# Performance work log

Measured on AMD Instinct MI355X. Metric: run time of the kernel, lower is better.

The kernel has to match this reference:

```python
import jax, jax.numpy as jnp
import numpy as np

UPPER = 0.4
LOWER = 0.1
BG_RATIO = 1.0
NCLS = 20
BACKGROUND = NCLS
SIGMA = 10.0          # SmoothL1Loss(10)
MAX_POS = 2048        # fixed capacity for positive RoIs (jit-friendly)
NEGATIVE = -2
NEITHER = -1


def bbox_overlaps(b1, b2):
    """Pairwise IoU, py-faster-rcnn +1 pixel convention. b1 [L,4], b2 [M,4] -> [L,M]."""
    a1 = (b1[:, 2] - b1[:, 0] + 1.0) * (b1[:, 3] - b1[:, 1] + 1.0)  # [L]
    a2 = (b2[:, 2] - b2[:, 0] + 1.0) * (b2[:, 3] - b2[:, 1] + 1.0)  # [M]
    iw = jnp.clip(jnp.minimum(b1[:, None, 2], b2[None, :, 2]) -
                  jnp.maximum(b1[:, None, 0], b2[None, :, 0]) + 1.0, 0.0)
    ih = jnp.clip(jnp.minimum(b1[:, None, 3], b2[None, :, 3]) -
                  jnp.maximum(b1[:, None, 1], b2[None, :, 1]) + 1.0, 0.0)
    inter = iw * ih
    return inter / (a1[:, None] + a2[None, :] - inter)


def smooth_l1(d):
    s2 = SIGMA * SIGMA
    ad = jnp.abs(d)
    return jnp.where(ad < 1.0 / s2, 0.5 * s2 * d * d, ad - 0.5 / s2)


def match(pred, gt):
    """Faithful port of match(): same assignment order (upper -> gt-argmax -> lower)."""
    L = pred.shape[0]
    M = gt.shape[0]
    ov = bbox_overlaps(pred, gt)                       # [L, M]
    best_p = ov.max(axis=1)
    idx_p = ov.argmax(axis=1).astype(jnp.int32)
    ret = jnp.full((L,), NEITHER, dtype=jnp.int32)
    ret = jnp.where(best_p >= UPPER, idx_p, ret)
    idx_g = ov.argmax(axis=0)                          # [M] best roi per gt
    ret = ret.at[idx_g].set(jnp.arange(M, dtype=jnp.int32))
    ret = jnp.where(best_p < LOWER, NEGATIVE, ret)     # applied last, as in torch
    return ret


def reference(rois, cls_scores, bbox_deltas, gt_boxes, gt_cls):
    L, C = cls_scores.shape
    boxes = rois[:, 1:]                                # drop batch index column
    score_idx = jnp.argmax(cls_scores, axis=1)         # [L] predicted class per roi
    deltas = bbox_deltas.reshape(L, C, 4)
    deltas = jnp.take_along_axis(deltas, score_idx[:, None, None], axis=1)[:, 0, :]
    pred = boxes + deltas                              # [L, 4]
    gt = gt_boxes[0]                                   # [M, 4]

    matches = match(pred, gt)                          # [L] int32
    pos = matches >= 0
    neg = matches == NEGATIVE
    num_pos = pos.sum()

    # --- negative sampling: randperm(neg)[:bg_num], done via random ranks ---
    bg_num = jnp.round(num_pos.astype(jnp.float32) * BG_RATIO).astype(jnp.int32)
    u = jax.random.uniform(jax.random.key(42), (L,))
    rank = jnp.zeros((L,), jnp.int32).at[jnp.argsort(jnp.where(neg, u, 2.0))].set(
        jnp.arange(L, dtype=jnp.int32))
    sel_neg = neg & (rank < bg_num)

    # --- classification loss (mean CE over pos + sampled neg) ---
    labels = jnp.where(pos, gt_cls[jnp.clip(matches, 0)], BACKGROUND)
    w = (pos | sel_neg).astype(cls_scores.dtype)
    logp = jax.nn.log_softmax(cls_scores, axis=1)
    ce = -jnp.take_along_axis(logp, labels[:, None], axis=1)[:, 0]
    cls_loss = (ce * w).sum() / w.sum()

    # --- bbox loss over positives (fixed-capacity gather) ---
    order = jnp.argsort(jnp.where(pos, jnp.arange(L), L + jnp.arange(L)))
    pos_idx = order[:MAX_POS]
    valid = pos[pos_idx].astype(pred.dtype)            # [K]
    pred_pos = pred[pos_idx]                           # [K, 4]
    gt_pos = gt[jnp.clip(matches[pos_idx], 0)]         # [K, 4]
    # original broadcasts pred [P,4] against gt.reshape(P,1,4) -> [P,P,4]
    diff = pred_pos[None, :, :] - gt_pos[:, None, :]   # [K, K, 4]
    pair_w = valid[:, None] * valid[None, :]
    bbox_loss = (smooth_l1(diff) * pair_w[:, :, None]).sum() / 1.0  # norm = ones(1)
    return cls_loss, bbox_loss


def setup_inputs() -> dict:
    key = jax.random.key(0)
    ks = jax.random.split(key, 6)
    L, C, M = 65536, 21, 512
    SCALE = 20000.0
    wh = jax.random.uniform(ks[0], (L, 2), minval=100.0, maxval=300.0)
    xy = jax.random.uniform(ks[1], (L, 2), minval=0.0, maxval=SCALE - 300.0)
    boxes = jnp.concatenate([xy, xy + wh], axis=1)                 # [L,4]
    rois = jnp.concatenate([jnp.zeros((L, 1)), boxes], axis=1)     # [L,5]
    jitter = jax.random.uniform(ks[2], (M, 4), minval=-10.0, maxval=10.0)
    gt_boxes = (boxes[:M] + jitter)[None]                          # [1,M,4], IoU>=0.4 w/ first M rois
    gt_cls = jax.random.randint(ks[3], (M,), 0, NCLS, dtype=jnp.int32)
    cls_scores = jax.random.normal(ks[4], (L, C))
    bbox_deltas = jax.random.normal(ks[5], (L, 4 * C)) * 2.0
    return dict(rois=rois, cls_scores=cls_scores, bbox_deltas=bbox_deltas,
                gt_boxes=gt_boxes, gt_cls=gt_cls)
```

## Files before the change

### kernel.cpp

```cpp
#include <hip/hip_runtime.h>
#include <stdint.h>

typedef unsigned int u32;
typedef unsigned long long u64;

#define F_UPPER 0.4f
#define F_LOWER 0.1f
#define MAX_POS 2048
#define L_SZ 65536
#define M_SZ 512
#define C_SZ 21
#define NBINS 8192
#define BIN_CAP 32
#define OVF_CAP 1024
#define COL_TAG 0xC000000000000000ull

struct State {
  int num_pos;
  int num_neg;
  u32 done;
  u32 _pad;
  double bbox_sum;
};

__device__ __forceinline__ float area_fn(const float4 a) {
#pragma clang fp contract(off)
  return (a.z - a.x + 1.0f) * (a.w - a.y + 1.0f);
}

__device__ __forceinline__ float iou_rcp(const float4 a, const float4 b, float a1, float a2) {
#pragma clang fp contract(off)
  float iw = fminf(a.z, b.z) - fmaxf(a.x, b.x) + 1.0f;
  iw = fmaxf(iw, 0.0f);
  float ih = fminf(a.w, b.w) - fmaxf(a.y, b.y) + 1.0f;
  ih = fmaxf(ih, 0.0f);
  float inter = iw * ih;
  return inter * __builtin_amdgcn_rcpf(a1 + a2 - inter);
}

__device__ __forceinline__ float sl1(float d) {
#pragma clang fp contract(off)
  float ad = fabsf(d);
  return (ad < 0.01f) ? (50.0f * d * d) : (ad - 0.005f);
}

__device__ __forceinline__ u32 rotl(u32 x, int d) { return (x << d) | (x >> (32 - d)); }

__device__ u32 threefry_bits(u32 i, u32 H) {
  u32 x0, x1; bool hi;
  if (i < H) { x0 = i;     x1 = i + H; hi = false; }
  else       { x0 = i - H; x1 = i;     hi = true;  }
  const u32 ks0 = 0u, ks1 = 42u;
  const u32 ks2 = ks0 ^ ks1 ^ 0x1BD11BDAu;
  x0 += ks0; x1 += ks1;
#define RND(r) { x0 += x1; x1 = rotl(x1, r); x1 ^= x0; }
  RND(13) RND(15) RND(26) RND(6)   x0 += ks1; x1 += ks2 + 1u;
  RND(17) RND(29) RND(16) RND(24)  x0 += ks2; x1 += ks0 + 2u;
  RND(13) RND(15) RND(26) RND(6)   x0 += ks0; x1 += ks1 + 3u;
  RND(17) RND(29) RND(16) RND(24)  x0 += ks1; x1 += ks2 + 4u;
  RND(13) RND(15) RND(26) RND(6)   x0 += ks2; x1 += ks0 + 5u;
#undef RND
  return hi ? x1 : x0;
}

__global__ void __launch_bounds__(256) kA(const float* __restrict__ rois,
    const float* __restrict__ scores, const float* __restrict__ deltas,
    const float4* __restrict__ gtb,
    float4* __restrict__ pred, float* __restrict__ lse,
    u64* __restrict__ rowkey, u64* __restrict__ gkey, u32* __restrict__ hist0) {
  __shared__ float  ssc[64 * C_SZ];
  __shared__ float  sro[64 * 5];
  __shared__ float4 sg[M_SZ];
  __shared__ float  ga[M_SZ];
  __shared__ u64    scol[M_SZ];
  __shared__ u64    srow[64];
  __shared__ float4 spred[64];
  __shared__ float  sarea[64];
  const int tid = threadIdx.x;
  const int pbase = blockIdx.x << 6;
  if (tid < 8) hist0[(blockIdx.x << 3) + tid] = 0u;
  for (int k = tid; k < 64 * C_SZ; k += 256) ssc[k] = scores[(size_t)pbase * C_SZ + k];
  for (int k = tid; k < 64 * 5; k += 256)    sro[k] = rois[(size_t)pbase * 5 + k];
  for (int j = tid; j < M_SZ; j += 256) {
    float4 g = gtb[j]; sg[j] = g; ga[j] = area_fn(g); scol[j] = 0ull;
  }
  if (tid < 64) srow[tid] = 0ull;
  __syncthreads();
  if (tid < 64) {
    const int i = pbase + tid;
    const float* sr = ssc + tid * C_SZ;
    float mx = sr[0]; int mi = 0;
    for (int j = 1; j < C_SZ; ++j) { float v = sr[j]; if (v > mx) { mx = v; mi = j; } }
    float s = 0.0f;
    for (int j = 0; j < C_SZ; ++j) s += expf(sr[j] - mx);
    lse[i] = mx + logf(s);
    float4 d = *(const float4*)(deltas + (size_t)i * (4 * C_SZ) + 4 * mi);
    const float* r = sro + tid * 5;
    float4 pb;
    pb.x = r[1] + d.x; pb.y = r[2] + d.y; pb.z = r[3] + d.z; pb.w = r[4] + d.w;
    spred[tid] = pb; sarea[tid] = area_fn(pb);
    pred[i] = pb;
  }
  __syncthreads();
  const int pg = tid & 7;
  const int gg = tid >> 3;
  const int p0 = pg << 3;
  float4 pb[8]; float pa[8]; float rbest[8]; int rbj[8];
#pragma unroll
  for (int r = 0; r < 8; ++r) {
    pb[r] = spred[p0 + r];
    pa[r] = sarea[p0 + r];
    rbest[r] = -1.0f;
    rbj[r] = 0;
  }
  const int jbase = gg << 4;
  const int joff = pg << 1;
#pragma unroll 2
  for (int jj = 0; jj < 16; ++jj) {
    const int j = jbase + ((jj + joff) & 15);
    const float4 gb = sg[j];
    const float gba = ga[j];
    float cbest = 0.0f; int cbp = 0;
#pragma unroll
    for (int r = 0; r < 8; ++r) {
      float v = iou_rcp(pb[r], gb, pa[r], gba);
      if (v > rbest[r]) { rbest[r] = v; rbj[r] = j; }
      if (v > cbest) { cbest = v; cbp = r; }
    }
    if (cbest > 0.0f) {
      u64 c = ((u64)__float_as_uint(cbest) << 32) |
              (u32)(0xFFFFFFFFu - (u32)(pbase + p0 + cbp));
      atomicMax(&scol[j], c);
    }
  }
#pragma unroll
  for (int r = 0; r < 8; ++r) {
    u64 k = ((u64)__float_as_uint(rbest[r]) << 32) | (u32)(0xFFFFFFFFu - (u32)rbj[r]);
    atomicMax(&srow[p0 + r], k);
  }
  __syncthreads();
  if (tid < 64) rowkey[pbase + tid] = srow[tid];
  for (int j = tid; j < M_SZ; j += 256) {
    u64 c = scol[j];
    if ((c >> 32) != 0ull) atomicMax(&gkey[j], c | COL_TAG);
  }
}

__global__ void __launch_bounds__(256) kB1(const u64* __restrict__ rowkey,
    const u64* __restrict__ gkey, const int* __restrict__ gtc,
    const float* __restrict__ scores, const float* __restrict__ lse,
    const float4* __restrict__ pred, const float4* __restrict__ gtb,
    u32* __restrict__ neg_u, u32* __restrict__ hist0, u64* __restrict__ bins,
    u32* __restrict__ blockcnt, double* __restrict__ posce,
    float4* __restrict__ ppg, float4* __restrict__ gpg) {
  __shared__ int sscat[256];
  __shared__ int swsum[4], sncnt[4];
  __shared__ double sdacc[4];
  const int tid = threadIdx.x, b = blockIdx.x;
  const int lane = tid & 63, wid = tid >> 6;
  sscat[tid] = -1;
  __syncthreads();
  for (int g = tid; g < M_SZ; g += 256) {
    u64 key = gkey[g];
    int pidx = (int)(0xFFFFFFFFu - (u32)key);
    if ((pidx >> 8) == b) atomicMax(&sscat[pidx & 255], g);
  }
  __syncthreads();
  const int i = (b << 8) + tid;
  u64 rk = rowkey[i];
  float best = __uint_as_float((u32)(rk >> 32));
  int idxp = (int)(0xFFFFFFFFu - (u32)rk);
  int m;
  if (best < F_LOWER) m = -2;
  else {
    int s = sscat[tid];
    m = (s >= 0) ? s : ((best >= F_UPPER) ? idxp : -1);
  }
  u32 ub = threefry_bits((u32)i, L_SZ >> 1) >> 9;
  neg_u[i] = (m == -2) ? ub : 0xFFFFFFFFu;
  float ce = 0.0f;
  if (m >= 0) {
    ce = lse[i] - scores[(size_t)i * C_SZ + gtc[m]];
  } else if (m == -2) {
    u32 bin = ub >> 10;
    u32 pos = atomicAdd(&hist0[bin], 1u);
    if (pos < BIN_CAP) bins[(size_t)bin * BIN_CAP + pos] = ((u64)ub << 16) | (u32)i;
  }
  const int flag = (m >= 0) ? 1 : 0;
  int incl = flag;
#pragma unroll
  for (int off = 1; off < 64; off <<= 1) {
    int x = __shfl_up(incl, off, 64);
    if (lane >= off) incl += x;
  }
  u64 baln = __ballot(m == -2);
  double acc = (double)ce;
  for (int off = 32; off > 0; off >>= 1) acc += __shfl_down(acc, off, 64);
  if (lane == 63) swsum[wid] = incl;
  if (lane == 0) { sncnt[wid] = __popcll(baln); sdacc[wid] = acc; }
  __syncthreads();
  int wbase = 0;
  for (int w = 0; w < wid; ++w) wbase += swsum[w];
  if (flag) {
    int lrank = wbase + incl - flag;
    ppg[(b << 8) + lrank] = pred[i];
    gpg[(b << 8) + lrank] = gtb[m];
  }
  if (tid == 0) {
    u32 cp = (u32)(swsum[0] + swsum[1] + swsum[2] + swsum[3]);
    u32 cn = (u32)(sncnt[0] + sncnt[1] + sncnt[2] + sncnt[3]);
    blockcnt[b] = cp | (cn << 16);
    posce[b] = sdacc[0] + sdacc[1] + sdacc[2] + sdacc[3];
  }
}

__global__ void __launch_bounds__(256) kB2(const float4* __restrict__ ppg,
    const float4* __restrict__ gpg,
    const u32* __restrict__ blockcnt, float4* __restrict__ pp, float4* __restrict__ gp,
    const u32* __restrict__ hist0, const u64* __restrict__ bins,
    const u32* __restrict__ neg_u, const float* __restrict__ scores,
    const float* __restrict__ lse, double* __restrict__ negce, State* st) {
  __shared__ int sscan[256];
  __shared__ int sncnt[4];
  __shared__ double sdacc[4];
  __shared__ int s_d, s_kk, s_cnt;
  __shared__ u32 s_ovf;
  __shared__ u64 sth;
  __shared__ u64 scand[OVF_CAP];
  const int tid = threadIdx.x, b = blockIdx.x;
  const int lane = tid & 63, wid = tid >> 6;
  u32 v = blockcnt[tid];
  int cp = (int)(v & 0xFFFFu), cn = (int)(v >> 16);
  sscan[tid] = cp;
  {
    int c = cn;
    for (int off = 32; off > 0; off >>= 1) c += __shfl_down(c, off, 64);
    if (lane == 0) sncnt[wid] = c;
  }
  __syncthreads();
  const int cnt_b = sscan[b];
  for (int off = 1; off < 256; off <<= 1) {
    int x = (tid >= off) ? sscan[tid - off] : 0;
    __syncthreads();
    sscan[tid] += x;
    __syncthreads();
  }
  const int bpref = (b == 0) ? 0 : sscan[b - 1];
  const int np = sscan[255];
  const int nn = sncnt[0] + sncnt[1] + sncnt[2] + sncnt[3];
  if (tid < cnt_b) {
    int rank = bpref + tid;
    if (rank < MAX_POS) {
      pp[rank] = ppg[(b << 8) + tid];
      gp[rank] = gpg[(b << 8) + tid];
    }
  }
  __syncthreads();
  u64 thresh = ~0ull;
  if (np < nn) {
    const uint4* h4 = (const uint4*)hist0;
    u32 loc[32]; int tsum = 0;
#pragma unroll
    for (int r = 0; r < 8; ++r) {
      uint4 hv = h4[tid * 8 + r];
      loc[r*4] = hv.x; loc[r*4+1] = hv.y; loc[r*4+2] = hv.z; loc[r*4+3] = hv.w;
      tsum += (int)(hv.x + hv.y + hv.z + hv.w);
    }
    sscan[tid] = tsum;
    __syncthreads();
    for (int off = 1; off < 256; off <<= 1) {
      int x = (tid >= off) ? sscan[tid - off] : 0;
      __syncthreads();
      sscan[tid] += x;
      __syncthreads();
    }
    int incl2 = sscan[tid], excl2 = incl2 - tsum;
    if (np >= excl2 && np < incl2) {
      int kk = np - excl2; int d = 0, c = 0;
#pragma unroll
      for (int r = 0; r < 32; ++r) {
        if (kk < (int)loc[r]) { d = tid * 32 + r; c = (int)loc[r]; break; }
        kk -= (int)loc[r];
      }
      s_d = d; s_kk = kk; s_cnt = c;
    }
    if (tid == 0) s_ovf = 0;
    __syncthreads();
    const int d = s_d, kk = s_kk, cnt = s_cnt;
    if (cnt <= BIN_CAP) {
      if (tid < cnt) scand[tid] = bins[(size_t)d * BIN_CAP + tid];
      __syncthreads();
      if (tid < cnt) {
        u64 key = scand[tid];
        int rank = 0;
        for (int u = 0; u < cnt; ++u) rank += (scand[u] < key) ? 1 : 0;
        if (rank == kk) sth = key;
      }
    } else {
      for (int t = tid; t < L_SZ; t += 256) {
        u32 u = neg_u[t];
        if (u != 0xFFFFFFFFu && (int)(u >> 10) == d) {
          u32 pos = atomicAdd(&s_ovf, 1u);
          if (pos < OVF_CAP) scand[pos] = ((u64)u << 16) | (u32)t;
        }
      }
      __syncthreads();
      int c2 = (int)s_ovf; if (c2 > OVF_CAP) c2 = OVF_CAP;
      for (int t = tid; t < c2; t += 256) {
        u64 key = scand[t];
        int rank = 0;
        for (int u = 0; u < c2; ++u) rank += (scand[u] < key) ? 1 : 0;
        if (rank == kk) sth = key;
      }
    }
    __syncthreads();
    thresh = sth;
  }
  const int i = (b << 8) + tid;
  u32 u = neg_u[i];
  double acc = 0.0;
  if (u != 0xFFFFFFFFu) {
    u64 key = ((u64)u << 16) | (u32)i;
    if (key < thresh)
      acc = (double)(lse[i] - scores[(size_t)i * C_SZ + (C_SZ - 1)]);
  }
  for (int off = 32; off > 0; off >>= 1) acc += __shfl_down(acc, off, 64);
  if (lane == 0) sdacc[wid] = acc;
  __syncthreads();
  if (tid == 0) {
    negce[b] = sdacc[0] + sdacc[1] + sdacc[2] + sdacc[3];
    if (b == 255) {
      st->num_pos = np; st->num_neg = nn;
      st->done = 0; st->bbox_sum = 0.0;
    }
  }
}

__global__ void __launch_bounds__(256) kC(const float4* __restrict__ pp,
    const float4* __restrict__ gp, const double* __restrict__ posce,
    const double* __restrict__ negce, State* st, float* __restrict__ out) {
  __shared__ float4 sj[128];
  __shared__ double sdacc[4];
  __shared__ int s_last;
  const int tid = threadIdx.x, b = blockIdx.x;
  const int lane = tid & 63, wid = tid >> 6;
  int n = st->num_pos; if (n > MAX_POS) n = MAX_POS;
  const int jb = (b & 15) << 7;
  if (tid < 128) {
    int j = jb + tid;
    sj[tid] = (j < n) ? pp[j] : make_float4(0.f, 0.f, 0.f, 0.f);
  }
  __syncthreads();
  const int ii = ((b >> 4) << 8) + tid;
  double pacc = 0.0;
  if (ii < n) {
    float4 g = gp[ii];
    int jend = n - jb; if (jend > 128) jend = 128;
    for (int j = 0; j < jend; ++j) {
      float4 p4 = sj[j];
      pacc += (double)sl1(p4.x - g.x);
      pacc += (double)sl1(p4.y - g.y);
      pacc += (double)sl1(p4.z - g.z);
      pacc += (double)sl1(p4.w - g.w);
    }
  }
  for (int off = 32; off > 0; off >>= 1) pacc += __shfl_down(pacc, off, 64);
  if (lane == 0) sdacc[wid] = pacc;
  __syncthreads();
  if (tid == 0) {
    atomicAdd(&st->bbox_sum, sdacc[0] + sdacc[1] + sdacc[2] + sdacc[3]);
    __threadfence();
    u32 dn = atomicAdd(&st->done, 1u);
    s_last = (dn == 127) ? 1 : 0;
  }
  __syncthreads();
  if (!s_last) return;
  double a = posce[tid] + negce[tid];
  for (int off = 32; off > 0; off >>= 1) a += __shfl_down(a, off, 64);
  if (lane == 0) sdacc[wid] = a;
  __syncthreads();
  if (tid == 0) {
    double ce = sdacc[0] + sdacc[1] + sdacc[2] + sdacc[3];
    double bbs = __hip_atomic_load(&st->bbox_sum, __ATOMIC_ACQUIRE, __HIP_MEMORY_SCOPE_AGENT);
    int np = st->num_pos, nn = st->num_neg;
    int nsel = (np < nn) ? np : nn;
    double wsum = (double)(np + nsel);
    out[0] = (float)(ce / wsum);
    out[1] = (float)bbs;
  }
}


extern "C" void kernel_launch(void* const* d_in, const int* in_sizes, int n_in,
                              void* d_out, int out_size, void* d_ws, size_t ws_size,
                              hipStream_t stream) {
  const float* rois   = (const float*)d_in[0];
  const float* scores = (const float*)d_in[1];
  const float* deltas = (const float*)d_in[2];
  const float4* gtb   = (const float4*)d_in[3];
  const int*   gtc    = (const int*)d_in[4];
  float* out = (float*)d_out;

  char* w = (char*)d_ws;
  State* st    = (State*)w;   w += 256;
  u64* gkey    = (u64*)w;     w += (size_t)M_SZ * 8;
  u32* hist0   = (u32*)w;     w += (size_t)NBINS * 4;
  u64* bins    = (u64*)w;     w += (size_t)NBINS * BIN_CAP * 8;
  float4* pred = (float4*)w;  w += (size_t)L_SZ * 16;
  float* lse   = (float*)w;   w += (size_t)L_SZ * 4;
  u64* rowkey  = (u64*)w;     w += (size_t)L_SZ * 8;
  u32* neg_u   = (u32*)w;     w += (size_t)L_SZ * 4;
  float4* ppg  = (float4*)w;  w += (size_t)256 * 256 * 16;
  float4* gpg  = (float4*)w;  w += (size_t)256 * 256 * 16;
  float4* pp   = (float4*)w;  w += (size_t)MAX_POS * 16;
  float4* gp   = (float4*)w;  w += (size_t)MAX_POS * 16;
  u32* blockcnt= (u32*)w;     w += 256 * 4;
  double* posce= (double*)w;  w += 256 * 8;
  double* negce= (double*)w;  w += 256 * 8;

  kA<<<L_SZ / 64, 256, 0, stream>>>(rois, scores, deltas, gtb, pred, lse, rowkey, gkey, hist0);
  kB1<<<L_SZ / 256, 256, 0, stream>>>(rowkey, gkey, gtc, scores, lse, pred, gtb,
                                      neg_u, hist0, bins, blockcnt, posce, ppg, gpg);
  kB2<<<L_SZ / 256, 256, 0, stream>>>(ppg, gpg, blockcnt, pp, gp,
                                      hist0, bins, neg_u, scores, lse, negce, st);
  kC<<<128, 256, 0, stream>>>(pp, gp, posce, negce, st, out);
}
```

Measured before the change: 130.7 us.

## Fuse post-match kernels into one cooperative kernel with grid syncs

Merges kB1, kB2 and kC into a single cooperative kernel that uses grid.sync between phases. This removes two kernel launches and the atomic last-block completion counter, and a deterministic final reduction replaces the atomic bbox sum. kA also gets vectorised float4 staging loads, computes GT areas inline, and skips the IoU divide and compare when the intersection is zero. The cooperative launch needs all 256 blocks resident at once, and grid syncs have their own cost.

```diff
diff --git a/kernel.cpp b/kernel.cpp
--- a/kernel.cpp
+++ b/kernel.cpp
@@ -1,5 +1,8 @@
 #include <hip/hip_runtime.h>
+#include <hip/hip_cooperative_groups.h>
 #include <stdint.h>
+
+namespace cg = cooperative_groups;
 
 typedef unsigned int u32;
 typedef unsigned long long u64;
@@ -15,26 +18,22 @@
 #define OVF_CAP 1024
 #define COL_TAG 0xC000000000000000ull
 
-struct State {
-  int num_pos;
-  int num_neg;
-  u32 done;
-  u32 _pad;
-  double bbox_sum;
-};
-
 __device__ __forceinline__ float area_fn(const float4 a) {
 #pragma clang fp contract(off)
   return (a.z - a.x + 1.0f) * (a.w - a.y + 1.0f);
 }
 
-__device__ __forceinline__ float iou_rcp(const float4 a, const float4 b, float a1, float a2) {
+__device__ __forceinline__ float inter_fn(const float4 a, const float4 b) {
 #pragma clang fp contract(off)
   float iw = fminf(a.z, b.z) - fmaxf(a.x, b.x) + 1.0f;
   iw = fmaxf(iw, 0.0f);
   float ih = fminf(a.w, b.w) - fmaxf(a.y, b.y) + 1.0f;
   ih = fmaxf(ih, 0.0f);
-  float inter = iw * ih;
+  return iw * ih;
+}
+
+__device__ __forceinline__ float iou_from_inter(float inter, float a1, float a2) {
+#pragma clang fp contract(off)
   return inter * __builtin_amdgcn_rcpf(a1 + a2 - inter);
 }
 
@@ -68,10 +67,9 @@
     const float4* __restrict__ gtb,
     float4* __restrict__ pred, float* __restrict__ lse,
     u64* __restrict__ rowkey, u64* __restrict__ gkey, u32* __restrict__ hist0) {
-  __shared__ float  ssc[64 * C_SZ];
-  __shared__ float  sro[64 * 5];
+  __shared__ __align__(16) float ssc[64 * C_SZ];
+  __shared__ __align__(16) float sro[64 * 5];
   __shared__ float4 sg[M_SZ];
-  __shared__ float  ga[M_SZ];
   __shared__ u64    scol[M_SZ];
   __shared__ u64    srow[64];
   __shared__ float4 spred[64];
@@ -79,10 +77,16 @@
   const int tid = threadIdx.x;
   const int pbase = blockIdx.x << 6;
   if (tid < 8) hist0[(blockIdx.x << 3) + tid] = 0u;
-  for (int k = tid; k < 64 * C_SZ; k += 256) ssc[k] = scores[(size_t)pbase * C_SZ + k];
-  for (int k = tid; k < 64 * 5; k += 256)    sro[k] = rois[(size_t)pbase * 5 + k];
+  {
+    const float4* s4 = (const float4*)(scores + (size_t)pbase * C_SZ);
+    float4* d4 = (float4*)ssc;
+    for (int k = tid; k < (64 * C_SZ) / 4; k += 256) d4[k] = s4[k];
+    const float4* r4 = (const float4*)(rois + (size_t)pbase * 5);
+    float4* q4 = (float4*)sro;
+    if (tid < (64 * 5) / 4) q4[tid] = r4[tid];
+  }
   for (int j = tid; j < M_SZ; j += 256) {
-    float4 g = gtb[j]; sg[j] = g; ga[j] = area_fn(g); scol[j] = 0ull;
+    float4 g = gtb[j]; sg[j] = g; scol[j] = 0ull;
   }
   if (tid < 64) srow[tid] = 0ull;
   __syncthreads();
@@ -110,22 +114,25 @@
   for (int r = 0; r < 8; ++r) {
     pb[r] = spred[p0 + r];
     pa[r] = sarea[p0 + r];
-    rbest[r] = -1.0f;
+    rbest[r] = 0.0f;
     rbj[r] = 0;
   }
   const int jbase = gg << 4;
-  const int joff = pg << 1;
+  const int joff = pg;
 #pragma unroll 2
   for (int jj = 0; jj < 16; ++jj) {
     const int j = jbase + ((jj + joff) & 15);
     const float4 gb = sg[j];
-    const float gba = ga[j];
+    const float gba = area_fn(gb);
     float cbest = 0.0f; int cbp = 0;
 #pragma unroll
     for (int r = 0; r < 8; ++r) {
-      float v = iou_rcp(pb[r], gb, pa[r], gba);
-      if (v > rbest[r]) { rbest[r] = v; rbj[r] = j; }
-      if (v > cbest) { cbest = v; cbp = r; }
+      float inter = inter_fn(pb[r], gb);
+      if (inter > 0.0f) {
+        float v = iou_from_inter(inter, pa[r], gba);
+        if (v > rbest[r]) { rbest[r] = v; rbj[r] = j; }
+        if (v > cbest) { cbest = v; cbp = r; }
+      }
     }
     if (cbest > 0.0f) {
       u64 c = ((u64)__float_as_uint(cbest) << 32) |
@@ -135,8 +142,10 @@
   }
 #pragma unroll
   for (int r = 0; r < 8; ++r) {
-    u64 k = ((u64)__float_as_uint(rbest[r]) << 32) | (u32)(0xFFFFFFFFu - (u32)rbj[r]);
-    atomicMax(&srow[p0 + r], k);
+    if (rbest[r] > 0.0f) {
+      u64 k = ((u64)__float_as_uint(rbest[r]) << 32) | (u32)(0xFFFFFFFFu - (u32)rbj[r]);
+      atomicMax(&srow[p0 + r], k);
+    }
   }
   __syncthreads();
   if (tid < 64) rowkey[pbase + tid] = srow[tid];
@@ -146,18 +155,29 @@
   }
 }
 
-__global__ void __launch_bounds__(256) kB1(const u64* __restrict__ rowkey,
-    const u64* __restrict__ gkey, const int* __restrict__ gtc,
-    const float* __restrict__ scores, const float* __restrict__ lse,
-    const float4* __restrict__ pred, const float4* __restrict__ gtb,
+__global__ void __launch_bounds__(256) kBC(
+    const u64* __restrict__ rowkey, const u64* __restrict__ gkey,
+    const int* __restrict__ gtc, const float* __restrict__ scores,
+    const float* __restrict__ lse, const float4* __restrict__ pred,
+    const float4* __restrict__ gtb,
     u32* __restrict__ neg_u, u32* __restrict__ hist0, u64* __restrict__ bins,
-    u32* __restrict__ blockcnt, double* __restrict__ posce,
-    float4* __restrict__ ppg, float4* __restrict__ gpg) {
+    u32* __restrict__ blockcnt, double* __restrict__ posce, double* __restrict__ negce,
+    float4* __restrict__ ppg, float4* __restrict__ gpg,
+    float4* __restrict__ pp, float4* __restrict__ gp,
+    double* __restrict__ bboxp, float* __restrict__ out) {
+  cg::grid_group grid = cg::this_grid();
   __shared__ int sscat[256];
   __shared__ int swsum[4], sncnt[4];
-  __shared__ double sdacc[4];
+  __shared__ double sdacc[4], sdbb[4];
+  __shared__ int sscan[256];
+  __shared__ int s_d, s_kk, s_cnt;
+  __shared__ u32 s_ovf;
+  __shared__ u64 sth;
+  __shared__ u64 scand[OVF_CAP];
+  __shared__ float4 sj[128];
   const int tid = threadIdx.x, b = blockIdx.x;
   const int lane = tid & 63, wid = tid >> 6;
+
   sscat[tid] = -1;
   __syncthreads();
   for (int g = tid; g < M_SZ; g += 256) {
@@ -177,7 +197,8 @@
     m = (s >= 0) ? s : ((best >= F_UPPER) ? idxp : -1);
   }
   u32 ub = threefry_bits((u32)i, L_SZ >> 1) >> 9;
-  neg_u[i] = (m == -2) ? ub : 0xFFFFFFFFu;
+  const u32 myu = (m == -2) ? ub : 0xFFFFFFFFu;
+  neg_u[i] = myu;
   float ce = 0.0f;
   if (m >= 0) {
     ce = lse[i] - scores[(size_t)i * C_SZ + gtc[m]];
@@ -186,207 +207,191 @@
     u32 pos = atomicAdd(&hist0[bin], 1u);
     if (pos < BIN_CAP) bins[(size_t)bin * BIN_CAP + pos] = ((u64)ub << 16) | (u32)i;
   }
-  const int flag = (m >= 0) ? 1 : 0;
-  int incl = flag;
-#pragma unroll
-  for (int off = 1; off < 64; off <<= 1) {
-    int x = __shfl_up(incl, off, 64);
-    if (lane >= off) incl += x;
-  }
-  u64 baln = __ballot(m == -2);
-  double acc = (double)ce;
-  for (int off = 32; off > 0; off >>= 1) acc += __shfl_down(acc, off, 64);
-  if (lane == 63) swsum[wid] = incl;
-  if (lane == 0) { sncnt[wid] = __popcll(baln); sdacc[wid] = acc; }
-  __syncthreads();
-  int wbase = 0;
-  for (int w = 0; w < wid; ++w) wbase += swsum[w];
-  if (flag) {
-    int lrank = wbase + incl - flag;
-    ppg[(b << 8) + lrank] = pred[i];
-    gpg[(b << 8) + lrank] = gtb[m];
-  }
-  if (tid == 0) {
-    u32 cp = (u32)(swsum[0] + swsum[1] + swsum[2] + swsum[3]);
-    u32 cn = (u32)(sncnt[0] + sncnt[1] + sncnt[2] + sncnt[3]);
-    blockcnt[b] = cp | (cn << 16);
-    posce[b] = sdacc[0] + sdacc[1] + sdacc[2] + sdacc[3];
-  }
-}
-
-__global__ void __launch_bounds__(256) kB2(const float4* __restrict__ ppg,
-    const float4* __restrict__ gpg,
-    const u32* __restrict__ blockcnt, float4* __restrict__ pp, float4* __restrict__ gp,
-    const u32* __restrict__ hist0, const u64* __restrict__ bins,
-    const u32* __restrict__ neg_u, const float* __restrict__ scores,
-    const float* __restrict__ lse, double* __restrict__ negce, State* st) {
-  __shared__ int sscan[256];
-  __shared__ int sncnt[4];
-  __shared__ double sdacc[4];
-  __shared__ int s_d, s_kk, s_cnt;
-  __shared__ u32 s_ovf;
-  __shared__ u64 sth;
-  __shared__ u64 scand[OVF_CAP];
-  const int tid = threadIdx.x, b = blockIdx.x;
-  const int lane = tid & 63, wid = tid >> 6;
-  u32 v = blockcnt[tid];
-  int cp = (int)(v & 0xFFFFu), cn = (int)(v >> 16);
-  sscan[tid] = cp;
   {
-    int c = cn;
-    for (int off = 32; off > 0; off >>= 1) c += __shfl_down(c, off, 64);
-    if (lane == 0) sncnt[wid] = c;
-  }
-  __syncthreads();
-  const int cnt_b = sscan[b];
-  for (int off = 1; off < 256; off <<= 1) {
-    int x = (tid >= off) ? sscan[tid - off] : 0;
+    const int flag = (m >= 0) ? 1 : 0;
+    int incl = flag;
+#pragma unroll
+    for (int off = 1; off < 64; off <<= 1) {
+      int x = __shfl_up(incl, off, 64);
+      if (lane >= off) incl += x;
+    }
+    u64 baln = __ballot(m == -2);
+    double acc = (double)ce;
+    for (int off = 32; off > 0; off >>= 1) acc += __shfl_down(acc, off, 64);
+    if (lane == 63) swsum[wid] = incl;
+    if (lane == 0) { sncnt[wid] = __popcll(baln); sdacc[wid] = acc; }
     __syncthreads();
-    sscan[tid] += x;
+    int wbase = 0;
+    for (int w = 0; w < wid; ++w) wbase += swsum[w];
+    if (flag) {
+      int lrank = wbase + incl - flag;
+      ppg[(b << 8) + lrank] = pred[i];
+      gpg[(b << 8) + lrank] = gtb[m];
+    }
+    if (tid == 0) {
+      u32 cp = (u32)(swsum[0] + swsum[1] + swsum[2] + swsum[3]);
+      u32 cn = (u32)(sncnt[0] + sncnt[1] + sncnt[2] + sncnt[3]);
+      blockcnt[b] = cp | (cn << 16);
+      posce[b] = sdacc[0] + sdacc[1] + sdacc[2] + sdacc[3];
+    }
+  }
+  __threadfence();
+  grid.sync();
+  __threadfence();
+
+  int np, nn, cnt_b, bpref;
+  {
+    u32 v = blockcnt[tid];
+    int cp = (int)(v & 0xFFFFu), cn = (int)(v >> 16);
+    sscan[tid] = cp;
+    {
+      int c = cn;
+      for (int off = 32; off > 0; off >>= 1) c += __shfl_down(c, off, 64);
+      if (lane == 0) sncnt[wid] = c;
+    }
     __syncthreads();
-  }
-  const int bpref = (b == 0) ? 0 : sscan[b - 1];
-  const int np = sscan[255];
-  const int nn = sncnt[0] + sncnt[1] + sncnt[2] + sncnt[3];
-  if (tid < cnt_b) {
-    int rank = bpref + tid;
-    if (rank < MAX_POS) {
-      pp[rank] = ppg[(b << 8) + tid];
-      gp[rank] = gpg[(b << 8) + tid];
-    }
-  }
-  __syncthreads();
-  u64 thresh = ~0ull;
-  if (np < nn) {
-    const uint4* h4 = (const uint4*)hist0;
-    u32 loc[32]; int tsum = 0;
-#pragma unroll
-    for (int r = 0; r < 8; ++r) {
-      uint4 hv = h4[tid * 8 + r];
-      loc[r*4] = hv.x; loc[r*4+1] = hv.y; loc[r*4+2] = hv.z; loc[r*4+3] = hv.w;
-      tsum += (int)(hv.x + hv.y + hv.z + hv.w);
-    }
-    sscan[tid] = tsum;
-    __syncthreads();
+    cnt_b = sscan[b];
     for (int off = 1; off < 256; off <<= 1) {
       int x = (tid >= off) ? sscan[tid - off] : 0;
       __syncthreads();
       sscan[tid] += x;
       __syncthreads();
     }
-    int incl2 = sscan[tid], excl2 = incl2 - tsum;
-    if (np >= excl2 && np < incl2) {
-      int kk = np - excl2; int d = 0, c = 0;
-#pragma unroll
-      for (int r = 0; r < 32; ++r) {
-        if (kk < (int)loc[r]) { d = tid * 32 + r; c = (int)loc[r]; break; }
-        kk -= (int)loc[r];
-      }
-      s_d = d; s_kk = kk; s_cnt = c;
-    }
-    if (tid == 0) s_ovf = 0;
+    bpref = (b == 0) ? 0 : sscan[b - 1];
+    np = sscan[255];
+    nn = sncnt[0] + sncnt[1] + sncnt[2] + sncnt[3];
+    if (tid < cnt_b) {
+      int rank = bpref + tid;
+      if (rank < MAX_POS) {
+        pp[rank] = ppg[(b << 8) + tid];
+        gp[rank] = gpg[(b << 8) + tid];
+      }
+    }
     __syncthreads();
-    const int d = s_d, kk = s_kk, cnt = s_cnt;
-    if (cnt <= BIN_CAP) {
-      if (tid < cnt) scand[tid] = bins[(size_t)d * BIN_CAP + tid];
-      __syncthreads();
-      if (tid < cnt) {
-        u64 key = scand[tid];
-        int rank = 0;
-        for (int u = 0; u < cnt; ++u) rank += (scand[u] < key) ? 1 : 0;
-        if (rank == kk) sth = key;
-      }
-    } else {
-      for (int t = tid; t < L_SZ; t += 256) {
-        u32 u = neg_u[t];
-        if (u != 0xFFFFFFFFu && (int)(u >> 10) == d) {
-          u32 pos = atomicAdd(&s_ovf, 1u);
-          if (pos < OVF_CAP) scand[pos] = ((u64)u << 16) | (u32)t;
+    u64 thresh = ~0ull;
+    if (np < nn) {
+      const uint4* h4 = (const uint4*)hist0;
+      u32 loc[32]; int tsum = 0;
+#pragma unroll
+      for (int r = 0; r < 8; ++r) {
+        uint4 hv = h4[tid * 8 + r];
+        loc[r*4] = hv.x; loc[r*4+1] = hv.y; loc[r*4+2] = hv.z; loc[r*4+3] = hv.w;
+        tsum += (int)(hv.x + hv.y + hv.z + hv.w);
+      }
+      sscan[tid] = tsum;
+      __syncthreads();
+      for (int off = 1; off < 256; off <<= 1) {
+        int x = (tid >= off) ? sscan[tid - off] : 0;
+        __syncthreads();
+        sscan[tid] += x;
+        __syncthreads();
+      }
+      int incl2 = sscan[tid], excl2 = incl2 - tsum;
+      if (np >= excl2 && np < incl2) {
+        int kk = np - excl2; int d = 0, c = 0;
+#pragma unroll
+        for (int r = 0; r < 32; ++r) {
+          if (kk < (int)loc[r]) { d = tid * 32 + r; c = (int)loc[r]; break; }
+          kk -= (int)loc[r];
         }
-      }
-      __syncthreads();
-      int c2 = (int)s_ovf; if (c2 > OVF_CAP) c2 = OVF_CAP;
-      for (int t = tid; t < c2; t += 256) {
-        u64 key = scand[t];
-        int rank = 0;
-        for (int u = 0; u < c2; ++u) rank += (scand[u] < key) ? 1 : 0;
-        if (rank == kk) sth = key;
-      }
-    }
+        s_d = d; s_kk = kk; s_cnt = c;
+      }
+      if (tid == 0) s_ovf = 0;
+      __syncthreads();
+      const int d = s_d, kk = s_kk, cnt = s_cnt;
+      if (cnt <= BIN_CAP) {
+        if (tid < cnt) scand[tid] = bins[(size_t)d * BIN_CAP + tid];
+        __syncthreads();
+        if (tid < cnt) {
+          u64 key = scand[tid];
+          int rank = 0;
+          for (int u = 0; u < cnt; ++u) rank += (scand[u] < key) ? 1 : 0;
+          if (rank == kk) sth = key;
+        }
+      } else {
+        for (int t = tid; t < L_SZ; t += 256) {
+          u32 u = neg_u[t];
+          if (u != 0xFFFFFFFFu && (int)(u >> 10) == d) {
+            u32 pos = atomicAdd(&s_ovf, 1u);
+            if (pos < OVF_CAP) scand[pos] = ((u64)u << 16) | (u32)t;
+          }
+        }
+        __syncthreads();
+        int c2 = (int)s_ovf; if (c2 > OVF_CAP) c2 = OVF_CAP;
+        for (int t = tid; t < c2; t += 256) {
+          u64 key = scand[t];
+          int rank = 0;
+          for (int u = 0; u < c2; ++u) rank += (scand[u] < key) ? 1 : 0;
+          if (rank == kk) sth = key;
+        }
+      }
+      __syncthreads();
+      thresh = sth;
+    }
+    double acc = 0.0;
+    if (myu != 0xFFFFFFFFu) {
+      u64 key = ((u64)myu << 16) | (u32)i;
+      if (key < thresh)
+        acc = (double)(lse[i] - scores[(size_t)i * C_SZ + (C_SZ - 1)]);
+    }
+    for (int off = 32; off > 0; off >>= 1) acc += __shfl_down(acc, off, 64);
+    if (lane == 0) sdacc[wid] = acc;
     __syncthreads();
-    thresh = sth;
-  }
-  const int i = (b << 8) + tid;
-  u32 u = neg_u[i];
-  double acc = 0.0;
-  if (u != 0xFFFFFFFFu) {
-    u64 key = ((u64)u << 16) | (u32)i;
-    if (key < thresh)
-      acc = (double)(lse[i] - scores[(size_t)i * C_SZ + (C_SZ - 1)]);
-  }
-  for (int off = 32; off > 0; off >>= 1) acc += __shfl_down(acc, off, 64);
-  if (lane == 0) sdacc[wid] = acc;
-  __syncthreads();
-  if (tid == 0) {
-    negce[b] = sdacc[0] + sdacc[1] + sdacc[2] + sdacc[3];
-    if (b == 255) {
-      st->num_pos = np; st->num_neg = nn;
-      st->done = 0; st->bbox_sum = 0.0;
-    }
-  }
-}
-
-__global__ void __launch_bounds__(256) kC(const float4* __restrict__ pp,
-    const float4* __restrict__ gp, const double* __restrict__ posce,
-    const double* __restrict__ negce, State* st, float* __restrict__ out) {
-  __shared__ float4 sj[128];
-  __shared__ double sdacc[4];
-  __shared__ int s_last;
-  const int tid = threadIdx.x, b = blockIdx.x;
-  const int lane = tid & 63, wid = tid >> 6;
-  int n = st->num_pos; if (n > MAX_POS) n = MAX_POS;
-  const int jb = (b & 15) << 7;
-  if (tid < 128) {
-    int j = jb + tid;
-    sj[tid] = (j < n) ? pp[j] : make_float4(0.f, 0.f, 0.f, 0.f);
-  }
-  __syncthreads();
-  const int ii = ((b >> 4) << 8) + tid;
-  double pacc = 0.0;
-  if (ii < n) {
-    float4 g = gp[ii];
-    int jend = n - jb; if (jend > 128) jend = 128;
-    for (int j = 0; j < jend; ++j) {
-      float4 p4 = sj[j];
-      pacc += (double)sl1(p4.x - g.x);
-      pacc += (double)sl1(p4.y - g.y);
-      pacc += (double)sl1(p4.z - g.z);
-      pacc += (double)sl1(p4.w - g.w);
-    }
-  }
-  for (int off = 32; off > 0; off >>= 1) pacc += __shfl_down(pacc, off, 64);
-  if (lane == 0) sdacc[wid] = pacc;
-  __syncthreads();
-  if (tid == 0) {
-    atomicAdd(&st->bbox_sum, sdacc[0] + sdacc[1] + sdacc[2] + sdacc[3]);
-    __threadfence();
-    u32 dn = atomicAdd(&st->done, 1u);
-    s_last = (dn == 127) ? 1 : 0;
-  }
-  __syncthreads();
-  if (!s_last) return;
-  double a = posce[tid] + negce[tid];
-  for (int off = 32; off > 0; off >>= 1) a += __shfl_down(a, off, 64);
-  if (lane == 0) sdacc[wid] = a;
-  __syncthreads();
-  if (tid == 0) {
-    double ce = sdacc[0] + sdacc[1] + sdacc[2] + sdacc[3];
-    double bbs = __hip_atomic_load(&st->bbox_sum, __ATOMIC_ACQUIRE, __HIP_MEMORY_SCOPE_AGENT);
-    int np = st->num_pos, nn = st->num_neg;
-    int nsel = (np < nn) ? np : nn;
-    double wsum = (double)(np + nsel);
-    out[0] = (float)(ce / wsum);
-    out[1] = (float)bbs;
+    if (tid == 0) negce[b] = sdacc[0] + sdacc[1] + sdacc[2] + sdacc[3];
+  }
+  __threadfence();
+  grid.sync();
+  __threadfence();
+
+  {
+    int n = np; if (n > MAX_POS) n = MAX_POS;
+    if (b < 128) {
+      const int jb = (b & 15) << 7;
+      if (tid < 128) {
+        int j = jb + tid;
+        sj[tid] = (j < n) ? pp[j] : make_float4(0.f, 0.f, 0.f, 0.f);
+      }
+      __syncthreads();
+      const int ii = ((b >> 4) << 8) + tid;
+      double pacc = 0.0;
+      if (ii < n) {
+        float4 g = gp[ii];
+        int jend = n - jb; if (jend > 128) jend = 128;
+        for (int j = 0; j < jend; ++j) {
+          float4 p4 = sj[j];
+          pacc += (double)sl1(p4.x - g.x);
+          pacc += (double)sl1(p4.y - g.y);
+          pacc += (double)sl1(p4.z - g.z);
+          pacc += (double)sl1(p4.w - g.w);
+        }
+      }
+      for (int off = 32; off > 0; off >>= 1) pacc += __shfl_down(pacc, off, 64);
+      if (lane == 0) sdacc[wid] = pacc;
+      __syncthreads();
+      if (tid == 0) bboxp[b] = sdacc[0] + sdacc[1] + sdacc[2] + sdacc[3];
+    }
+  }
+  __threadfence();
+  grid.sync();
+  __threadfence();
+
+  if (b == 0) {
+    double a = posce[tid] + negce[tid];
+    double bb = (tid < 128) ? bboxp[tid] : 0.0;
+    for (int off = 32; off > 0; off >>= 1) {
+      a += __shfl_down(a, off, 64);
+      bb += __shfl_down(bb, off, 64);
+    }
+    if (lane == 0) { sdacc[wid] = a; sdbb[wid] = bb; }
+    __syncthreads();
+    if (tid == 0) {
+      double cesum = sdacc[0] + sdacc[1] + sdacc[2] + sdacc[3];
+      double bbs = sdbb[0] + sdbb[1] + sdbb[2] + sdbb[3];
+      int nsel = (np < nn) ? np : nn;
+      double wsum = (double)(np + nsel);
+      out[0] = (float)(cesum / wsum);
+      out[1] = (float)bbs;
+    }
   }
 }
 
@@ -402,7 +407,6 @@
   float* out = (float*)d_out;
 
   char* w = (char*)d_ws;
-  State* st    = (State*)w;   w += 256;
   u64* gkey    = (u64*)w;     w += (size_t)M_SZ * 8;
   u32* hist0   = (u32*)w;     w += (size_t)NBINS * 4;
   u64* bins    = (u64*)w;     w += (size_t)NBINS * BIN_CAP * 8;
@@ -417,11 +421,12 @@
   u32* blockcnt= (u32*)w;     w += 256 * 4;
   double* posce= (double*)w;  w += 256 * 8;
   double* negce= (double*)w;  w += 256 * 8;
+  double* bboxp= (double*)w;  w += 128 * 8;
 
   kA<<<L_SZ / 64, 256, 0, stream>>>(rois, scores, deltas, gtb, pred, lse, rowkey, gkey, hist0);
-  kB1<<<L_SZ / 256, 256, 0, stream>>>(rowkey, gkey, gtc, scores, lse, pred, gtb,
-                                      neg_u, hist0, bins, blockcnt, posce, ppg, gpg);
-  kB2<<<L_SZ / 256, 256, 0, stream>>>(ppg, gpg, blockcnt, pp, gp,
-                                      hist0, bins, neg_u, scores, lse, negce, st);
-  kC<<<128, 256, 0, stream>>>(pp, gp, posce, negce, st, out);
-}
+
+  void* args[] = {&rowkey, &gkey, &gtc, &scores, &lse, &pred, &gtb,
+                  &neg_u, &hist0, &bins, &blockcnt, &posce, &negce,
+                  &ppg, &gpg, &pp, &gp, &bboxp, &out};
+  (void)hipLaunchCooperativeKernel((void*)kBC, dim3(256), dim3(256), args, 0, stream);
+}
```

Result: slower. 297.0 us (+127.2%).
